# Performance work log

Measured on AMD Instinct MI355X. Metric: run time of the kernel, lower is better.

## Reference

```python
import jax, jax.numpy as jnp
import numpy as np

N_HEAD = 16

def _rope_cache(dim, T):
    # matches precompute_rope_cache: angles = outer(pos, 1/theta^(2i/dim))
    pos = jnp.arange(T, dtype=jnp.float32)
    freq = 1.0 / (10000.0 ** (jnp.arange(0, dim, 2, dtype=jnp.float32) / dim))
    ang = pos[:, None] * freq[None, :]  # (T, dim//2)
    return jnp.cos(ang), jnp.sin(ang)

def _apply_rope(x, cos, sin):
    # x: (B, H, T, hs). Faithful to the (nonstandard, roll-based) torch apply_rope,
    # including the reassignment of x_rot before it is used for x_pass.
    x_rot, x_pass = x[..., ::2], x[..., 1::2]
    c = cos[None, None]  # (1,1,T,hs//2)
    s = sin[None, None]
    new_rot = x_rot * c - jnp.roll(x_pass, 1, axis=-1) * s
    new_pass = x_pass * c + jnp.roll(new_rot, -1, axis=-1) * s
    return jnp.stack([new_rot, new_pass], axis=-1).reshape(x.shape)

def setup_inputs() -> dict:
    key = jax.random.key(0)
    k1, k2, k3 = jax.random.split(key, 3)
    B, T, C = 2, 2048, 1024
    x = jax.random.normal(k1, (B, T, C), dtype=jnp.float32)
    w_attn = jax.random.normal(k2, (3 * C, C), dtype=jnp.float32) * 0.02
    w_proj = jax.random.normal(k3, (C, C), dtype=jnp.float32) * 0.02
    return {"x": x, "w_attn": w_attn, "w_proj": w_proj}

def reference(x, w_attn, w_proj):
    B, T, C = x.shape
    H = N_HEAD
    hs = C // H
    qkv = jnp.einsum('btc,dc->btd', x, w_attn)  # fused QKV projection (no bias)
    q, k, v = jnp.split(qkv, 3, axis=-1)
    def heads(t):
        return t.reshape(B, T, H, hs).transpose(0, 2, 1, 3)  # (B,H,T,hs)
    q, k, v = heads(q), heads(k), heads(v)
    cos, sin = _rope_cache(hs, T)
    q = _apply_rope(q, cos, sin)
    k = _apply_rope(k, cos, sin)
    scores = jnp.einsum('bhqd,bhkd->bhqk', q, k) / jnp.sqrt(jnp.float32(hs))
    causal = jnp.tril(jnp.ones((T, T), dtype=bool))
    scores = jnp.where(causal[None, None], scores, -jnp.inf)
    att = jax.nn.softmax(scores, axis=-1)
    y = jnp.einsum('bhqk,bhkd->bhqd', att, v)
    y = y.transpose(0, 2, 1, 3).reshape(B, T, C)
    return jnp.einsum('btc,dc->btd', y, w_proj)
```

## Files before the change

kernel.cpp:

```cpp
#include <hip/hip_runtime.h>

#define T_SEQ 2048
#define NHEAD 16
#define HS 64

typedef __bf16 bf16x8 __attribute__((ext_vector_type(8)));
typedef float f32x4 __attribute__((ext_vector_type(4)));

__device__ __forceinline__ unsigned short f2bf(float f) {
  union { float f; unsigned int u; } v; v.f = f;
  return (unsigned short)((v.u + 0x7fffu + ((v.u >> 16) & 1u)) >> 16);
}
__device__ __forceinline__ float bf2f(unsigned short h) {
  union { unsigned int u; float f; } v; v.u = ((unsigned int)h) << 16;
  return v.f;
}
__device__ __forceinline__ bf16x8 ld_bf8(const unsigned short* p) {
  return *(const bf16x8*)p;
}
__device__ __forceinline__ void st_bf8(unsigned short* p, bf16x8 v) {
  *(bf16x8*)p = v;
}
__device__ __forceinline__ bf16x8 cvt8(float4 a, float4 b) {
  bf16x8 r;
  r[0] = (__bf16)a.x; r[1] = (__bf16)a.y; r[2] = (__bf16)a.z; r[3] = (__bf16)a.w;
  r[4] = (__bf16)b.x; r[5] = (__bf16)b.y; r[6] = (__bf16)b.z; r[7] = (__bf16)b.w;
  return r;
}
__device__ __forceinline__ void gload_lds16(const void* g, void* l) {
  __builtin_amdgcn_global_load_lds(
      (const __attribute__((address_space(1))) unsigned int*)g,
      (__attribute__((address_space(3))) unsigned int*)l, 16, 0, 0);
}

__global__ __launch_bounds__(256) void cvt_bf16(const float* __restrict__ src,
                                                unsigned short* __restrict__ dst) {
  const size_t i = ((size_t)blockIdx.x * 256 + threadIdx.x) * 8;
  const float4 a = *(const float4*)(src + i);
  const float4 b = *(const float4*)(src + i + 4);
  st_bf8(dst + i, cvt8(a, b));
}

__global__ __launch_bounds__(256, 2) void gemm_bt(
    const unsigned short* __restrict__ A, const void* __restrict__ Bv,
    float* __restrict__ Cout,
    unsigned short* __restrict__ qb, unsigned short* __restrict__ kb,
    unsigned short* __restrict__ vtb,
    int M, int N, int K, int bf32, int mode) {
  __shared__ unsigned short As[128 * 64];
  __shared__ unsigned short Bs[128 * 64];
  const int tid = threadIdx.x;
  const int wid = tid >> 6, lane = tid & 63;
  const int quad = lane >> 4, l16 = lane & 15;
  const int m0 = blockIdx.y * 128, n0 = blockIdx.x * 128;
  const int wm = (wid >> 1) * 64, wn = (wid & 1) * 64;
  const int srow = lane >> 3;
  const int scol = (lane & 7) * 8;
  const int brow = tid >> 3;
  const int bcol = (tid & 7) * 8;
  const unsigned short* Bh = (const unsigned short*)Bv;
  const float* Bf = (const float*)Bv;
  f32x4 acc[4][4] = {};
  const int nkt = K >> 6;
  for (int kt = 0; kt < nkt; ++kt) {
    const int k0 = kt * 64;
    #pragma unroll
    for (int j = 0; j < 4; ++j) {
      const int rr = wid * 32 + j * 8 + srow;
      gload_lds16(A + (size_t)(m0 + rr) * K + k0 + scol,
                  &As[(wid * 32 + j * 8) * 64]);
    }
    if (bf32) {
      bf16x8 bs8[4];
      #pragma unroll
      for (int j = 0; j < 4; ++j) {
        const float* p = Bf + (size_t)(n0 + j * 32 + brow) * K + k0 + bcol;
        bs8[j] = cvt8(*(const float4*)p, *(const float4*)(p + 4));
      }
      #pragma unroll
      for (int j = 0; j < 4; ++j)
        st_bf8(&Bs[(j * 32 + brow) * 64 + bcol], bs8[j]);
    } else {
      #pragma unroll
      for (int j = 0; j < 4; ++j) {
        const int rr = wid * 32 + j * 8 + srow;
        gload_lds16(Bh + (size_t)(n0 + rr) * K + k0 + scol,
                    &Bs[(wid * 32 + j * 8) * 64]);
      }
    }
    __syncthreads();
    #pragma unroll
    for (int ks = 0; ks < 2; ++ks) {
      bf16x8 af[4], bfr[4];
      #pragma unroll
      for (int mt = 0; mt < 4; ++mt)
        af[mt] = ld_bf8(&As[(wm + mt * 16 + l16) * 64 + ks * 32 + quad * 8]);
      #pragma unroll
      for (int nt = 0; nt < 4; ++nt)
        bfr[nt] = ld_bf8(&Bs[(wn + nt * 16 + l16) * 64 + ks * 32 + quad * 8]);
      #pragma unroll
      for (int mt = 0; mt < 4; ++mt)
        #pragma unroll
        for (int nt = 0; nt < 4; ++nt)
          acc[mt][nt] = __builtin_amdgcn_mfma_f32_16x16x32_bf16(af[mt], bfr[nt], acc[mt][nt], 0, 0, 0);
    }
    __syncthreads();
  }
  #pragma unroll
  for (int mt = 0; mt < 4; ++mt) {
    #pragma unroll
    for (int nt = 0; nt < 4; ++nt) {
      const int n = n0 + wn + nt * 16 + l16;
      #pragma unroll
      for (int r = 0; r < 4; ++r) {
        const int m = m0 + wm + mt * 16 + quad * 4 + r;
        if (mode == 0) {
          Cout[(size_t)m * N + n] = acc[mt][nt][r];
        } else {
          const unsigned short val = f2bf(acc[mt][nt][r]);
          const int b = m >> 11, t = m & (T_SEQ - 1);
          const int which = n >> 10, c = n & 1023;
          const int h = c >> 6, d = c & 63;
          const int bh = b * NHEAD + h;
          if (which == 0)      qb[((size_t)bh * T_SEQ + t) * HS + d] = val;
          else if (which == 1) kb[((size_t)bh * T_SEQ + t) * HS + d] = val;
          else                 vtb[((size_t)bh * HS + d) * T_SEQ + t] = val;
        }
      }
    }
  }
}

__global__ __launch_bounds__(256, 1) void rope(unsigned short* __restrict__ qb,
                                               unsigned short* __restrict__ kb) {
  const int idx = blockIdx.x * 256 + threadIdx.x;
  unsigned short* buf = (idx < 65536 ? qb : kb) + (size_t)(idx & 65535) * HS;
  const int t = idx & (T_SEQ - 1);
  float x[64];
  #pragma unroll
  for (int j = 0; j < 64; ++j) x[j] = bf2f(buf[j]);
  __asm__ volatile("" ::: "memory");
  float c[32], s[32], er[32];
  #pragma unroll
  for (int i = 0; i < 32; ++i) {
    const float ang = (float)t * exp2f(-0.41524101186092029f * (float)i);
    c[i] = cosf(ang); s[i] = sinf(ang);
  }
  #pragma unroll
  for (int i = 0; i < 32; ++i)
    er[i] = x[2 * i] * c[i] - x[(2 * i + 63) & 63] * s[i];
  #pragma unroll
  for (int i = 0; i < 32; ++i) {
    const float ep = x[2 * i + 1] * c[i] + er[(i + 1) & 31] * s[i];
    buf[2 * i]     = f2bf(er[i]);
    buf[2 * i + 1] = f2bf(ep);
  }
}

__global__ __launch_bounds__(256) void attn(
    const unsigned short* __restrict__ qb, const unsigned short* __restrict__ kb,
    const unsigned short* __restrict__ vt, unsigned short* __restrict__ yb) {
  __shared__ __bf16 Pl[4][16][72];
  const int wid = threadIdx.x >> 6;
  const int u = blockIdx.x * 4 + wid;
  const int qi = 127 - (u >> 5);
  const int bh = u & 31;
  const int q0 = qi * 16;
  const int lane = threadIdx.x & 63;
  const int quad = lane >> 4, l16 = lane & 15;

  const unsigned short* qptr = qb + ((size_t)bh * T_SEQ + q0 + l16) * HS;
  const bf16x8 aq0 = ld_bf8(qptr + quad * 8);
  const bf16x8 aq1 = ld_bf8(qptr + 32 + quad * 8);
  f32x4 O[4] = {};
  float m_i[4], l_i[4], alpha[4];
  #pragma unroll
  for (int r = 0; r < 4; ++r) { m_i[r] = -1e30f; l_i[r] = 0.f; }

  const unsigned short* kbase = kb + (size_t)bh * T_SEQ * HS;
  const unsigned short* vbase = vt + (size_t)bh * HS * T_SEQ;
  const int kend = q0 + 15;

  for (int k0 = 0; k0 <= kend; k0 += 64) {
    bf16x8 bk[4][2];
    #pragma unroll
    for (int t = 0; t < 4; ++t) {
      const unsigned short* kp = kbase + (size_t)(k0 + t * 16 + l16) * HS;
      bk[t][0] = ld_bf8(kp + quad * 8);
      bk[t][1] = ld_bf8(kp + 32 + quad * 8);
    }
    f32x4 S[4] = {};
    __builtin_amdgcn_s_setprio(1);
    #pragma unroll
    for (int t = 0; t < 4; ++t) {
      S[t] = __builtin_amdgcn_mfma_f32_16x16x32_bf16(aq0, bk[t][0], S[t], 0, 0, 0);
      S[t] = __builtin_amdgcn_mfma_f32_16x16x32_bf16(aq1, bk[t][1], S[t], 0, 0, 0);
    }
    __builtin_amdgcn_s_setprio(0);
    bf16x8 vb[2][4];
    #pragma unroll
    for (int c = 0; c < 2; ++c)
      #pragma unroll
      for (int vg = 0; vg < 4; ++vg)
        vb[c][vg] = ld_bf8(vbase + (size_t)(vg * 16 + l16) * T_SEQ + k0 + c * 32 + quad * 8);
    #pragma unroll
    for (int r = 0; r < 4; ++r) {
      const int row = q0 + quad * 4 + r;
      float s[4];
      #pragma unroll
      for (int t = 0; t < 4; ++t)
        s[t] = (k0 + t * 16 + l16 <= row) ? S[t][r] * 0.125f : -1e30f;
      float tm = fmaxf(fmaxf(s[0], s[1]), fmaxf(s[2], s[3]));
      #pragma unroll
      for (int off = 1; off < 16; off <<= 1) tm = fmaxf(tm, __shfl_xor(tm, off, 64));
      const float mnew = fmaxf(m_i[r], tm);
      alpha[r] = __expf(m_i[r] - mnew);
      unsigned short h[4];
      float rs = 0.f;
      #pragma unroll
      for (int t = 0; t < 4; ++t) {
        h[t] = f2bf(__expf(s[t] - mnew));
        rs += bf2f(h[t]);
      }
      #pragma unroll
      for (int off = 1; off < 16; off <<= 1) rs += __shfl_xor(rs, off, 64);
      l_i[r] = l_i[r] * alpha[r] + rs;
      m_i[r] = mnew;
      #pragma unroll
      for (int t = 0; t < 4; ++t)
        Pl[wid][quad * 4 + r][t * 16 + l16] = __builtin_bit_cast(__bf16, h[t]);
    }
    #pragma unroll
    for (int vg = 0; vg < 4; ++vg)
      #pragma unroll
      for (int r = 0; r < 4; ++r) O[vg][r] *= alpha[r];
    __builtin_amdgcn_s_setprio(1);
    #pragma unroll
    for (int c = 0; c < 2; ++c) {
      const bf16x8 pa = *(const bf16x8*)&Pl[wid][l16][c * 32 + quad * 8];
      #pragma unroll
      for (int vg = 0; vg < 4; ++vg)
        O[vg] = __builtin_amdgcn_mfma_f32_16x16x32_bf16(pa, vb[c][vg], O[vg], 0, 0, 0);
    }
    __builtin_amdgcn_s_setprio(0);
  }
  const int b = bh >> 4, h = bh & 15;
  #pragma unroll
  for (int r = 0; r < 4; ++r) {
    const float inv = 1.0f / fmaxf(l_i[r], 1e-30f);
    const int row = q0 + quad * 4 + r;
    #pragma unroll
    for (int vg = 0; vg < 4; ++vg)
      yb[((size_t)b * T_SEQ + row) * 1024 + h * HS + vg * 16 + l16] = f2bf(O[vg][r] * inv);
  }
}

extern "C" void kernel_launch(void* const* d_in, const int* in_sizes, int n_in,
                              void* d_out, int out_size, void* d_ws, size_t ws_size,
                              hipStream_t stream) {
  const float* x      = (const float*)d_in[0];
  const float* w_attn = (const float*)d_in[1];
  const float* w_proj = (const float*)d_in[2];
  float* out = (float*)d_out;
  unsigned short* qb = (unsigned short*)d_ws;
  unsigned short* kb = qb + (size_t)4194304;
  unsigned short* vt = kb + (size_t)4194304;
  unsigned short* yb = vt + (size_t)4194304;
  unsigned short* xb = yb;
  unsigned short* wab = yb + (size_t)4194304;
  unsigned short* wpb = wab + (size_t)3145728;
  const int big = ws_size >= (size_t)40 * 1024 * 1024;

  cvt_bf16<<<dim3(2048), 256, 0, stream>>>(x, xb);
  if (big) {
    cvt_bf16<<<dim3(1536), 256, 0, stream>>>(w_attn, wab);
    cvt_bf16<<<dim3(512), 256, 0, stream>>>(w_proj, wpb);
  }
  if (big)
    gemm_bt<<<dim3(24, 32), 256, 0, stream>>>(xb, wab, nullptr, qb, kb, vt,
                                              4096, 3072, 1024, 0, 1);
  else
    gemm_bt<<<dim3(24, 32), 256, 0, stream>>>(xb, w_attn, nullptr, qb, kb, vt,
                                              4096, 3072, 1024, 1, 1);
  rope<<<dim3(512), 256, 0, stream>>>(qb, kb);
  attn<<<dim3(1024), 256, 0, stream>>>(qb, kb, vt, yb);
  if (big)
    gemm_bt<<<dim3(8, 32), 256, 0, stream>>>(yb, wpb, out, nullptr, nullptr, nullptr,
                                             4096, 1024, 1024, 0, 0);
  else
    gemm_bt<<<dim3(8, 32), 256, 0, stream>>>(yb, w_proj, out, nullptr, nullptr, nullptr,
                                             4096, 1024, 1024, 1, 0);
}
```

Measured before the change: 296.8 us.

## Split attention KV range across two blocks and merge partials in combine kernel

The causal attention kernel's KV loop is split in half across a new grid dimension. Each half writes unnormalized fp32 partial outputs plus per-row max and sum to workspace, and a new combine kernel merges the two with log-sum-exp rescaling and writes bf16 output. The aim is to double the wave count and shorten the longest per-wave critical path for late query tiles. In exchange it adds an extra kernel launch and substantial fp32 partial-result traffic. It is only used when the workspace is at least 74 MB.

New measurement: 307.1 us. 3.5% more time.

```diff
diff --git a/kernel.cpp b/kernel.cpp
--- a/kernel.cpp
+++ b/kernel.cpp
@@ -159,13 +159,21 @@
 
 __global__ __launch_bounds__(256) void attn(
     const unsigned short* __restrict__ qb, const unsigned short* __restrict__ kb,
-    const unsigned short* __restrict__ vt, unsigned short* __restrict__ yb) {
+    const unsigned short* __restrict__ vt, unsigned short* __restrict__ yb,
+    float* __restrict__ Op, float* __restrict__ ml, int split) {
   __shared__ __bf16 Pl[4][16][72];
   const int wid = threadIdx.x >> 6;
   const int u = blockIdx.x * 4 + wid;
   const int qi = 127 - (u >> 5);
   const int bh = u & 31;
   const int q0 = qi * 16;
+  const int np = (qi >> 2) + 1;
+  int p0 = 0, p1 = np;
+  if (split) {
+    const int half = np >> 1;
+    if (blockIdx.y == 0) p1 = half;
+    else                 p0 = half;
+  }
   const int lane = threadIdx.x & 63;
   const int quad = lane >> 4, l16 = lane & 15;
 
@@ -179,9 +187,9 @@
 
   const unsigned short* kbase = kb + (size_t)bh * T_SEQ * HS;
   const unsigned short* vbase = vt + (size_t)bh * HS * T_SEQ;
-  const int kend = q0 + 15;
-
-  for (int k0 = 0; k0 <= kend; k0 += 64) {
+
+  for (int p = p0; p < p1; ++p) {
+    const int k0 = p * 64;
     bf16x8 bk[4][2];
     #pragma unroll
     for (int t = 0; t < 4; ++t) {
@@ -244,14 +252,52 @@
     }
     __builtin_amdgcn_s_setprio(0);
   }
+  if (!split) {
+    const int b = bh >> 4, h = bh & 15;
+    #pragma unroll
+    for (int r = 0; r < 4; ++r) {
+      const float inv = 1.0f / fmaxf(l_i[r], 1e-30f);
+      const int row = q0 + quad * 4 + r;
+      #pragma unroll
+      for (int vg = 0; vg < 4; ++vg)
+        yb[((size_t)b * T_SEQ + row) * 1024 + h * HS + vg * 16 + l16] = f2bf(O[vg][r] * inv);
+    }
+  } else {
+    const size_t base = ((size_t)blockIdx.y * 32 + bh) * T_SEQ;
+    #pragma unroll
+    for (int r = 0; r < 4; ++r) {
+      const int row = q0 + quad * 4 + r;
+      #pragma unroll
+      for (int vg = 0; vg < 4; ++vg)
+        Op[(base + row) * 64 + vg * 16 + l16] = O[vg][r];
+      if (l16 == 0) {
+        ml[(base + row) * 2]     = m_i[r];
+        ml[(base + row) * 2 + 1] = l_i[r];
+      }
+    }
+  }
+}
+
+__global__ __launch_bounds__(64) void combine(const float* __restrict__ Op,
+                                              const float* __restrict__ ml,
+                                              unsigned short* __restrict__ yb) {
+  const int w = blockIdx.x;
+  const int bh = w >> 7;
+  const int t0 = (w & 127) * 16;
+  const int lane = threadIdx.x;
   const int b = bh >> 4, h = bh & 15;
-  #pragma unroll
-  for (int r = 0; r < 4; ++r) {
-    const float inv = 1.0f / fmaxf(l_i[r], 1e-30f);
-    const int row = q0 + quad * 4 + r;
-    #pragma unroll
-    for (int vg = 0; vg < 4; ++vg)
-      yb[((size_t)b * T_SEQ + row) * 1024 + h * HS + vg * 16 + l16] = f2bf(O[vg][r] * inv);
+  const size_t s0 = (size_t)bh * T_SEQ;
+  const size_t s1 = (size_t)(32 + bh) * T_SEQ;
+  for (int r = 0; r < 16; ++r) {
+    const int t = t0 + r;
+    const float m0 = ml[(s0 + t) * 2], l0 = ml[(s0 + t) * 2 + 1];
+    const float m1 = ml[(s1 + t) * 2], l1 = ml[(s1 + t) * 2 + 1];
+    const float m = fmaxf(m0, m1);
+    const float a0 = __expf(m0 - m), a1 = __expf(m1 - m);
+    const float l = l0 * a0 + l1 * a1;
+    const float o = Op[(s0 + t) * 64 + lane] * a0 +
+                    Op[(s1 + t) * 64 + lane] * a1;
+    yb[((size_t)b * T_SEQ + t) * 1024 + h * HS + lane] = f2bf(o / fmaxf(l, 1e-30f));
   }
 }
 
@@ -269,25 +315,27 @@
   unsigned short* xb = yb;
   unsigned short* wab = yb + (size_t)4194304;
   unsigned short* wpb = wab + (size_t)3145728;
-  const int big = ws_size >= (size_t)40 * 1024 * 1024;
+  float* Opart = (float*)((char*)d_ws + ((size_t)40 << 20));
+  float* mlb   = (float*)((char*)d_ws + ((size_t)72 << 20));
+  const int bigw = ws_size >= ((size_t)40 << 20);
+  const int bigs = ws_size >= ((size_t)74 << 20);
 
   cvt_bf16<<<dim3(2048), 256, 0, stream>>>(x, xb);
-  if (big) {
+  if (bigw) {
     cvt_bf16<<<dim3(1536), 256, 0, stream>>>(w_attn, wab);
     cvt_bf16<<<dim3(512), 256, 0, stream>>>(w_proj, wpb);
   }
-  if (big)
-    gemm_bt<<<dim3(24, 32), 256, 0, stream>>>(xb, wab, nullptr, qb, kb, vt,
-                                              4096, 3072, 1024, 0, 1);
-  else
-    gemm_bt<<<dim3(24, 32), 256, 0, stream>>>(xb, w_attn, nullptr, qb, kb, vt,
-                                              4096, 3072, 1024, 1, 1);
+  gemm_bt<<<dim3(24, 32), 256, 0, stream>>>(
+      xb, bigw ? (const void*)wab : (const void*)w_attn, nullptr,
+      qb, kb, vt, 4096, 3072, 1024, bigw ? 0 : 1, 1);
   rope<<<dim3(512), 256, 0, stream>>>(qb, kb);
-  attn<<<dim3(1024), 256, 0, stream>>>(qb, kb, vt, yb);
-  if (big)
-    gemm_bt<<<dim3(8, 32), 256, 0, stream>>>(yb, wpb, out, nullptr, nullptr, nullptr,
-                                             4096, 1024, 1024, 0, 0);
-  else
-    gemm_bt<<<dim3(8, 32), 256, 0, stream>>>(yb, w_proj, out, nullptr, nullptr, nullptr,
-                                             4096, 1024, 1024, 1, 0);
-}
+  if (bigs) {
+    attn<<<dim3(1024, 2), 256, 0, stream>>>(qb, kb, vt, nullptr, Opart, mlb, 1);
+    combine<<<dim3(4096), 64, 0, stream>>>(Opart, mlb, yb);
+  } else {
+    attn<<<dim3(1024), 256, 0, stream>>>(qb, kb, vt, yb, nullptr, nullptr, 0);
+  }
+  gemm_bt<<<dim3(8, 32), 256, 0, stream>>>(
+      yb, bigw ? (const void*)wpb : (const void*)w_proj, out,
+      nullptr, nullptr, nullptr, 4096, 1024, 1024, bigw ? 0 : 1, 0);
+}
```
